# Kernel tuning notes

Measured on AMD Instinct MI355X. Metric: run time of the kernel, lower is better.

## Reference

```python
import jax, jax.numpy as jnp
import numpy as np

B, M, C = 8, 1024, 4096
OP_DIM, MACH_DIM, HID = 128, 128, 128
LEAKY_SLOPE = 0.01  # torch LeakyReLU default


def setup_inputs() -> dict:
    key = jax.random.key(0)
    ks = jax.random.split(key, 10)
    s = lambda *sh: 1.0 / np.sqrt(sh[0])
    return {
        "operation_features": jax.random.normal(ks[0], (B, C, OP_DIM), jnp.float32),
        "machine_features": jax.random.normal(ks[1], (B, M, MACH_DIM), jnp.float32),
        "type_match_mask": jax.random.randint(ks[2], (B, M, C), 0, 2).astype(jnp.float32),
        "q_w": jax.random.uniform(ks[3], (MACH_DIM, HID), jnp.float32, -s(MACH_DIM), s(MACH_DIM)),
        "q_b": jax.random.uniform(ks[4], (HID,), jnp.float32, -s(MACH_DIM), s(MACH_DIM)),
        "kv_w": jax.random.uniform(ks[5], (OP_DIM, 2 * HID), jnp.float32, -s(OP_DIM), s(OP_DIM)),
        "kv_b": jax.random.uniform(ks[6], (2 * HID,), jnp.float32, -s(OP_DIM), s(OP_DIM)),
        "score_w": jax.random.uniform(ks[7], (2 * HID, 1), jnp.float32, -s(2 * HID), s(2 * HID)),
        "score_b": jax.random.uniform(ks[8], (1,), jnp.float32, -s(2 * HID), s(2 * HID)),
        "out_w": jax.random.uniform(ks[9], (HID, MACH_DIM), jnp.float32, -s(HID), s(HID)),
        "out_b": jnp.zeros((MACH_DIM,), jnp.float32),
    }


def reference(operation_features, machine_features, type_match_mask,
              q_w, q_b, kv_w, kv_b, score_w, score_b, out_w, out_b):
    H = q_w.shape[1]
    q = machine_features @ q_w + q_b                      # [B, M, H]
    kv = operation_features @ kv_w + kv_b                 # [B, C, 2H]
    k, v = kv[..., :H], kv[..., H:]                       # [B, C, H] each
    # score MLP Linear(2H -> 1) on cat([q, k]) == q @ Wq + k @ Wk + b,
    # broadcast over [B, M, C] -> never materialize the [B, M, C, 2H] concat.
    wq, wk = score_w[:H, 0], score_w[H:, 0]
    scores = (q @ wq)[:, :, None] + (k @ wk)[:, None, :] + score_b[0]  # [B, M, C]
    scores = jnp.where(scores >= 0, scores, LEAKY_SLOPE * scores)     # LeakyReLU
    masked = scores * type_match_mask                                  # multiplicative mask (as in source)
    attn = jax.nn.softmax(masked, axis=-1)                             # softmax over operations C
    weighted = jnp.einsum('bmc,bch->bmh', attn, v)                     # [B, M, H]
    return weighted @ out_w + out_b                                    # [B, M, MACH_DIM]
```

## Files before the change

### kernel.cpp

```cpp
#include <hip/hip_runtime.h>
#include <hip/hip_bf16.h>

typedef __attribute__((ext_vector_type(8))) short short8;
typedef __attribute__((ext_vector_type(8))) unsigned short u16x8;
typedef __attribute__((ext_vector_type(4))) unsigned short u16x4;
typedef __attribute__((ext_vector_type(4))) float f32x4;
typedef __attribute__((ext_vector_type(4))) unsigned int u32x4;

#define L2E 1.44269504f

__device__ __forceinline__ unsigned short f2bf(float f){
  unsigned u = __float_as_uint(f);
  u += 0x7fffu + ((u >> 16) & 1u);
  return (unsigned short)(u >> 16);
}
__device__ __forceinline__ unsigned pk_bf16(float lo, float hi){
  unsigned a = __float_as_uint(lo);
  a += 0x7fffu + ((a >> 16) & 1u);
  unsigned b = __float_as_uint(hi);
  b += 0x7fffu + ((b >> 16) & 1u);
  return (a >> 16) | (b & 0xffff0000u);
}

__global__ void prep_vecs(const float* __restrict__ qw, const float* __restrict__ qb,
                          const float* __restrict__ kvw, const float* __restrict__ kvb,
                          const float* __restrict__ scw, const float* __restrict__ scb,
                          float* __restrict__ qv, float* __restrict__ kvv,
                          float* __restrict__ cqck){
  int d = threadIdx.x;
  const float4* qr = (const float4*)(qw + d*128);
  const float4* kr = (const float4*)(kvw + d*256);
  float a = 0.f, c = 0.f;
  #pragma unroll 8
  for (int i = 0; i < 32; ++i){
    float4 q4 = qr[i];
    float4 w4 = *(const float4*)(scw + i*4);
    a = fmaf(q4.x, w4.x, a); a = fmaf(q4.y, w4.y, a);
    a = fmaf(q4.z, w4.z, a); a = fmaf(q4.w, w4.w, a);
    float4 k4 = kr[i];
    float4 v4 = *(const float4*)(scw + 128 + i*4);
    c = fmaf(k4.x, v4.x, c); c = fmaf(k4.y, v4.y, c);
    c = fmaf(k4.z, v4.z, c); c = fmaf(k4.w, v4.w, c);
  }
  qv[d] = a; kvv[d] = c;
  if (d == 0){
    float cq = scb[0], ck = 0.f;
    #pragma unroll 8
    for (int i = 0; i < 32; ++i){
      float4 qb4 = *(const float4*)(qb + i*4);
      float4 w4  = *(const float4*)(scw + i*4);
      float4 kb4 = *(const float4*)(kvb + i*4);
      float4 v4  = *(const float4*)(scw + 128 + i*4);
      cq = fmaf(qb4.x, w4.x, cq); cq = fmaf(qb4.y, w4.y, cq);
      cq = fmaf(qb4.z, w4.z, cq); cq = fmaf(qb4.w, w4.w, cq);
      ck = fmaf(kb4.x, v4.x, ck); ck = fmaf(kb4.y, v4.y, ck);
      ck = fmaf(kb4.z, v4.z, ck); ck = fmaf(kb4.w, v4.w, ck);
    }
    cqck[0] = cq; cqck[1] = ck;
  }
}

__global__ __launch_bounds__(256) void prep_w2(const float* __restrict__ kvw,
                          const float* __restrict__ kvb,
                          const float* __restrict__ outw, const float* __restrict__ outb,
                          unsigned short* __restrict__ w2t, float* __restrict__ c2){
  int blk = blockIdx.x;
  if (blk < 64){
    int idx = blk*256 + threadIdx.x;
    int di = idx >> 7, ho = idx & 127;
    const float* kr = kvw + di*256 + 128;
    float s = 0.f;
    for (int h = 0; h < 128; ++h) s = fmaf(kr[h], outw[h*128 + ho], s);
    w2t[ho*128 + di] = f2bf(s);
  } else if (threadIdx.x < 128){
    int ho = threadIdx.x;
    float s = outb[ho];
    for (int h = 0; h < 128; ++h) s = fmaf(kvb[128 + h], outw[h*128 + ho], s);
    c2[ho] = s;
  }
}

__global__ __launch_bounds__(256) void prep_sq(const float* __restrict__ mf,
                          const float* __restrict__ qv, const float* __restrict__ cqck,
                          float* __restrict__ sqp){
  int row = blockIdx.x*4 + (threadIdx.x >> 6);
  int lane = threadIdx.x & 63;
  float s = mf[row*128 + lane] * qv[lane] + mf[row*128 + 64 + lane] * qv[64 + lane];
  #pragma unroll
  for (int o = 32; o; o >>= 1) s += __shfl_xor(s, o, 64);
  if (lane == 0) sqp[row] = L2E * (s + cqck[0]);
}

__global__ __launch_bounds__(256) void prep_sk_tr(const float* __restrict__ of,
                          const float* __restrict__ kvv, const float* __restrict__ cqck,
                          float* __restrict__ skp, unsigned short* __restrict__ ofTk){
  __shared__ unsigned short tile[64*130];
  int b  = blockIdx.x >> 6;
  int c0 = (blockIdx.x & 63) << 6;
  int t  = threadIdx.x;
  int r  = t >> 2, dq = (t & 3) << 5;
  const float* src = of + ((size_t)(b*4096 + c0 + r))*128 + dq;
  float part = 0.f;
  #pragma unroll
  for (int j = 0; j < 32; j += 4){
    float4 v = *(const float4*)(src + j);
    part = fmaf(v.x, kvv[dq + j],     part);
    part = fmaf(v.y, kvv[dq + j + 1], part);
    part = fmaf(v.z, kvv[dq + j + 2], part);
    part = fmaf(v.w, kvv[dq + j + 3], part);
    tile[r*130 + dq + j]     = f2bf(v.x);
    tile[r*130 + dq + j + 1] = f2bf(v.y);
    tile[r*130 + dq + j + 2] = f2bf(v.z);
    tile[r*130 + dq + j + 3] = f2bf(v.w);
  }
  part += __shfl_xor(part, 1, 64);
  part += __shfl_xor(part, 2, 64);
  if ((t & 3) == 0) skp[b*4096 + c0 + r] = L2E * (part + cqck[1]);
  __syncthreads();
  int d = t >> 1, chh = (t & 1) << 5;
  #pragma unroll
  for (int j = 0; j < 4; ++j){
    int cg = c0 + chh + j*8;
    int ksg = cg >> 5, l4g = (cg >> 3) & 3;
    u16x8 v;
    #pragma unroll
    for (int k = 0; k < 8; ++k) v[k] = tile[(chh + j*8 + k)*130 + d];
    *(u16x8*)(ofTk + (((size_t)(b*128 + ksg)*4 + l4g)*128 + d)*8) = v;
  }
}


#define ISSUE_M(MS, KS) { M##MS##a = *(const float4*)(mbase + (KS)*32);          \
                          M##MS##b = *(const float4*)(mbase + (KS)*32 + 4); }
#define ISSUE_S(SS, KS) { S##SS##a = *(const float4*)(sbase + (KS)*32);          \
                          S##SS##b = *(const float4*)(sbase + (KS)*32 + 4); }
#define ISSUE_B(BS, KS) {                                                        \
  const unsigned short* bp = bbase + (size_t)(KS)*4096;                          \
  B##BS##_0 = *(const short8*)(bp);        B##BS##_1 = *(const short8*)(bp+128); \
  B##BS##_2 = *(const short8*)(bp+256);    B##BS##_3 = *(const short8*)(bp+384); \
  B##BS##_4 = *(const short8*)(bp+512);    B##BS##_5 = *(const short8*)(bp+640); \
  B##BS##_6 = *(const short8*)(bp+768);    B##BS##_7 = *(const short8*)(bp+896); }

#define KSTEP(KS, MS, BS, PFB, PFM)                                              \
{                                                                                \
  float sx[8] = {S##BS##a.x,S##BS##a.y,S##BS##a.z,S##BS##a.w,                    \
                 S##BS##b.x,S##BS##b.y,S##BS##b.z,S##BS##b.w};                   \
  float mx[8] = {M##MS##a.x,M##MS##a.y,M##MS##a.z,M##MS##a.w,                    \
                 M##MS##b.x,M##MS##b.y,M##MS##b.z,M##MS##b.w};                   \
  float pv[8];                                                                   \
  _Pragma("unroll")                                                              \
  for (int j = 0; j < 8; ++j){                                                   \
    float s = sqv + sx[j];                  \
    s = fmaxf(s, 0.01f*s);                   \
    s *= mx[j];                                        \
    pv[j] = __builtin_amdgcn_exp2f(s);                                           \
  }                                                                              \
  u32x4 pk;                                                                      \
  pk[0] = pk_bf16(pv[0], pv[1]);                                                 \
  pk[1] = pk_bf16(pv[2], pv[3]);                                                 \
  pk[2] = pk_bf16(pv[4], pv[5]);                                                 \
  pk[3] = pk_bf16(pv[6], pv[7]);                                                 \
  short8 pa = __builtin_bit_cast(short8, pk);                                    \
  accS = __builtin_amdgcn_mfma_f32_16x16x32_bf16(pa, ones, accS, 0, 0, 0);       \
  acc0 = __builtin_amdgcn_mfma_f32_16x16x32_bf16(pa, B##BS##_0, acc0, 0, 0, 0);  \
  acc1 = __builtin_amdgcn_mfma_f32_16x16x32_bf16(pa, B##BS##_1, acc1, 0, 0, 0);  \
  acc2 = __builtin_amdgcn_mfma_f32_16x16x32_bf16(pa, B##BS##_2, acc2, 0, 0, 0);  \
  acc3 = __builtin_amdgcn_mfma_f32_16x16x32_bf16(pa, B##BS##_3, acc3, 0, 0, 0);  \
  acc4 = __builtin_amdgcn_mfma_f32_16x16x32_bf16(pa, B##BS##_4, acc4, 0, 0, 0);  \
  acc5 = __builtin_amdgcn_mfma_f32_16x16x32_bf16(pa, B##BS##_5, acc5, 0, 0, 0);  \
  acc6 = __builtin_amdgcn_mfma_f32_16x16x32_bf16(pa, B##BS##_6, acc6, 0, 0, 0);  \
  acc7 = __builtin_amdgcn_mfma_f32_16x16x32_bf16(pa, B##BS##_7, acc7, 0, 0, 0);  \
  if (PFB){ ISSUE_B(BS, (KS)+2); ISSUE_S(BS, (KS)+2); }                          \
  if (PFM){ ISSUE_M(MS, (KS)+4); }                                              \
}

template<int CSL2>
__global__ __launch_bounds__(256, 2) void attn_main(
    const float* __restrict__ mask, const float* __restrict__ sqp,
    const float* __restrict__ skp, const unsigned short* __restrict__ ofTk,
    float* __restrict__ pacc, float* __restrict__ prs)
{
  constexpr int CS = 1 << CSL2;
  constexpr int NK = 128 >> CSL2;
  const int t = threadIdx.x, w = t >> 6, l = t & 63;
  const int l15 = l & 15, l4 = l >> 4;
  const int unit = blockIdx.x*4 + w;
  const int cs   = unit & (CS - 1);
  const int bmt  = unit >> CSL2;
  const int b    = bmt >> 6;
  const int m0   = (bmt & 63) << 4;
  const int c0   = cs << (12 - CSL2);

  const int grow = b*1024 + m0 + l15;
  const float sqv = sqp[grow];
  const float* mbase = mask + (size_t)grow*4096 + c0 + l4*8;
  const float* sbase = skp + b*4096 + c0 + l4*8;
  const unsigned short* bbase =
      ofTk + (((size_t)(b*128 + (c0 >> 5))*4 + l4)*128 + l15)*8;

  const short one_bf = (short)0x3F80;
  const short8 ones = {one_bf,one_bf,one_bf,one_bf,one_bf,one_bf,one_bf,one_bf};

  f32x4 acc0={0,0,0,0},acc1={0,0,0,0},acc2={0,0,0,0},acc3={0,0,0,0},
        acc4={0,0,0,0},acc5={0,0,0,0},acc6={0,0,0,0},acc7={0,0,0,0},
        accS={0,0,0,0};
  float4 M0a,M0b,M1a,M1b,M2a,M2b,M3a,M3b;
  float4 S0a,S0b,S1a,S1b;
  short8 B0_0,B0_1,B0_2,B0_3,B0_4,B0_5,B0_6,B0_7;
  short8 B1_0,B1_1,B1_2,B1_3,B1_4,B1_5,B1_6,B1_7;

  ISSUE_M(0, 0); ISSUE_S(0, 0);
  ISSUE_B(0, 0);
  ISSUE_M(1, 1); ISSUE_S(1, 1);
  ISSUE_B(1, 1);
  ISSUE_M(2, 2); ISSUE_M(3, 3);

  for (int g = 0; g < NK/4 - 1; ++g){
    const int ks = g*4;
    KSTEP(ks+0, 0, 0, true, true);
    KSTEP(ks+1, 1, 1, true, true);
    KSTEP(ks+2, 2, 0, true, true);
    KSTEP(ks+3, 3, 1, true, true);
  }
  KSTEP(NK-4, 0, 0, true,  false);
  KSTEP(NK-3, 1, 1, true,  false);
  KSTEP(NK-2, 2, 0, false, false);
  KSTEP(NK-1, 3, 1, false, false);

  if (l15 == 0) *(f32x4*)(prs + unit*16 + l4*4) = accS;

  float* po = pacc + (size_t)unit*2048 + l15*16 + l4*4;
  *(f32x4*)(po + 0*256) = acc0;  *(f32x4*)(po + 1*256) = acc1;
  *(f32x4*)(po + 2*256) = acc2;  *(f32x4*)(po + 3*256) = acc3;
  *(f32x4*)(po + 4*256) = acc4;  *(f32x4*)(po + 5*256) = acc5;
  *(f32x4*)(po + 6*256) = acc6;  *(f32x4*)(po + 7*256) = acc7;
}

__global__ __launch_bounds__(256) void reduce_gemm2(
    const float* __restrict__ pacc, const float* __restrict__ prs,
    const unsigned short* __restrict__ w2t, const float* __restrict__ c2,
    float* __restrict__ out, int csl2)
{
  __shared__ unsigned short A2[64*128];
  __shared__ float rs[64];
  const int bmt64 = blockIdx.x;
  const int b = bmt64 >> 4, mt = bmt64 & 15;
  const int CS = 1 << csl2;
  const int t = threadIdx.x;

  f32x4 a[8];
  #pragma unroll
  for (int i = 0; i < 8; ++i) a[i] = {0.f,0.f,0.f,0.f};
  for (int cs = 0; cs < CS; ++cs){
    #pragma unroll
    for (int i = 0; i < 8; ++i){
      const int flat = (i*256 + t)*4;
      const int q = flat >> 11, f2 = flat & 2047;
      const float* pb = pacc + ((size_t)((bmt64*4 + q)*CS + cs))*2048 + f2;
      f32x4 v = *(const f32x4*)pb;
      a[i][0]+=v[0]; a[i][1]+=v[1]; a[i][2]+=v[2]; a[i][3]+=v[3];
    }
  }
  if (t < 64){
    float s = 0.f;
    const int q = t >> 4, r16 = t & 15;
    for (int cs = 0; cs < CS; ++cs) s += prs[((bmt64*4 + q)*CS + cs)*16 + r16];
    rs[t] = 1.f / s;
  }
  __syncthreads();
  #pragma unroll
  for (int i = 0; i < 8; ++i){
    const int flat = (i*256 + t)*4;
    const int q = flat >> 11, f2 = flat & 2047;
    const int col = f2 >> 4, r16 = f2 & 15;
    #pragma unroll
    for (int k = 0; k < 4; ++k){
      const int row = q*16 + r16 + k;
      unsigned short h = f2bf(a[i][k] * rs[row]);
      *(unsigned short*)((char*)A2 + row*256 + ((col*2) ^ ((row & 7) << 4))) = h;
    }
  }
  __syncthreads();

  const int w = t >> 6, l = t & 63, l15 = l & 15, l4 = l >> 4;
  f32x4 o[4][2];
  #pragma unroll
  for (int mf = 0; mf < 4; ++mf){ o[mf][0] = {0.f,0.f,0.f,0.f}; o[mf][1] = {0.f,0.f,0.f,0.f}; }
  const unsigned short* wp0 = w2t + (size_t)(w*32 + l15)*128 + l4*8;
  const char* ab = (const char*)A2 + l15*256;
  const int xa = (l15 & 7) << 4;
  #pragma unroll
  for (int ks = 0; ks < 4; ++ks){
    short8 b0 = *(const short8*)(wp0 + ks*32);
    short8 b1 = *(const short8*)(wp0 + 16*128 + ks*32);
    #pragma unroll
    for (int mf = 0; mf < 4; ++mf){
      short8 af = *(const short8*)(ab + mf*4096 + ((ks*64 + l4*16) ^ xa));
      o[mf][0] = __builtin_amdgcn_mfma_f32_16x16x32_bf16(af, b0, o[mf][0], 0, 0, 0);
      o[mf][1] = __builtin_amdgcn_mfma_f32_16x16x32_bf16(af, b1, o[mf][1], 0, 0, 0);
    }
  }
  #pragma unroll
  for (int mf = 0; mf < 4; ++mf)
    #pragma unroll
    for (int n = 0; n < 2; ++n){
      const int col = w*32 + n*16 + l15;
      const float cc = c2[col];
      #pragma unroll
      for (int j = 0; j < 4; ++j){
        const int row = mf*16 + l4*4 + j;
        out[((size_t)(b*1024 + mt*64 + row))*128 + col] = o[mf][n][j] + cc;
      }
    }
}

extern "C" void kernel_launch(void* const* d_in, const int* in_sizes, int n_in,
                              void* d_out, int out_size, void* d_ws, size_t ws_size,
                              hipStream_t stream){
  const float* of   = (const float*)d_in[0];
  const float* mf   = (const float*)d_in[1];
  const float* mask = (const float*)d_in[2];
  const float* qw   = (const float*)d_in[3];
  const float* qb   = (const float*)d_in[4];
  const float* kvw  = (const float*)d_in[5];
  const float* kvb  = (const float*)d_in[6];
  const float* scw  = (const float*)d_in[7];
  const float* scb  = (const float*)d_in[8];
  const float* outw = (const float*)d_in[9];
  const float* outb = (const float*)d_in[10];
  float* out = (float*)d_out;

  char* ws = (char*)d_ws;
  unsigned short* ofTk = (unsigned short*)(ws);
  unsigned short* w2t  = (unsigned short*)(ws + 8388608);
  float* c2   = (float*)(ws + 8421376);
  float* sqp  = (float*)(ws + 8421888);
  float* skp  = (float*)(ws + 8454656);
  float* qv   = (float*)(ws + 8585728);
  float* kvv  = (float*)(ws + 8586240);
  float* cqck = (float*)(ws + 8586752);
  const size_t fixed_end = 8587008;

  int csl2 = 2;
  while (csl2 > 1){
    size_t nunit = (size_t)512 << csl2;
    if (fixed_end + nunit*16*4 + nunit*2048*4 <= ws_size) break;
    --csl2;
  }
  size_t nunit = (size_t)512 << csl2;
  float* prs  = (float*)(ws + fixed_end);
  float* pacc = (float*)(ws + fixed_end + nunit*16*4);
  int nblk = (int)(nunit >> 2);

  prep_vecs<<<1, 128, 0, stream>>>(qw, qb, kvw, kvb, scw, scb, qv, kvv, cqck);
  prep_w2<<<65, 256, 0, stream>>>(kvw, kvb, outw, outb, w2t, c2);
  prep_sq<<<2048, 256, 0, stream>>>(mf, qv, cqck, sqp);
  prep_sk_tr<<<512, 256, 0, stream>>>(of, kvv, cqck, skp, ofTk);
  if (csl2 == 2)
    attn_main<2><<<nblk, 256, 0, stream>>>(mask, sqp, skp, ofTk, pacc, prs);
  else
    attn_main<1><<<nblk, 256, 0, stream>>>(mask, sqp, skp, ofTk, pacc, prs);
  reduce_gemm2<<<128, 256, 0, stream>>>(pacc, prs, w2t, c2, out, csl2);
}
```

Before: 75.87 us.

## Stream mask and key scores through LDS via async global-to-LDS loads

The main attention kernel now stages the mask tiles in a 4-deep per-wave LDS ring and the per-column key scores in LDS, filled with global_load_lds direct copies and paced by explicit vmcnt waits. The B operand is loaded per step instead of double-buffered in registers, which frees registers so occupancy can go from 2 to 4 blocks per CU. The column split is raised from 4 to 8 slices, which gives more units and more partial results to reduce. The risks are fragile hand-tuned waitcnt values, extra LDS traffic, and a larger partial-sum buffer and reduction.

```diff
diff --git a/kernel.cpp b/kernel.cpp
--- a/kernel.cpp
+++ b/kernel.cpp
@@ -20,6 +20,11 @@
   unsigned b = __float_as_uint(hi);
   b += 0x7fffu + ((b >> 16) & 1u);
   return (a >> 16) | (b & 0xffff0000u);
+}
+__device__ __forceinline__ void gl_lds16(const void* g, void* l){
+  __builtin_amdgcn_global_load_lds(
+      (const __attribute__((address_space(1))) unsigned*)g,
+      (__attribute__((address_space(3))) unsigned*)l, 16, 0, 0);
 }
 
 __global__ void prep_vecs(const float* __restrict__ qw, const float* __restrict__ qb,
@@ -130,23 +135,30 @@
 }
 
 
-#define ISSUE_M(MS, KS) { M##MS##a = *(const float4*)(mbase + (KS)*32);          \
-                          M##MS##b = *(const float4*)(mbase + (KS)*32 + 4); }
-#define ISSUE_S(SS, KS) { S##SS##a = *(const float4*)(sbase + (KS)*32);          \
-                          S##SS##b = *(const float4*)(sbase + (KS)*32 + 4); }
-#define ISSUE_B(BS, KS) {                                                        \
+#define WVAL(KS) ((KS)==0 ? 0 : (KS)==1 ? 10 : (KS)==2 ? 20 : \
+                  ((KS) >= NK-3 ? (24 + 2*(NK-1-(KS))) : 30))
+
+#define KSTEP(KS) if ((KS) < NK) {                                               \
+  asm volatile("s_waitcnt vmcnt(%0)" :: "i"(WVAL(KS)) : "memory");               \
+  __builtin_amdgcn_sched_barrier(0);                                             \
   const unsigned short* bp = bbase + (size_t)(KS)*4096;                          \
-  B##BS##_0 = *(const short8*)(bp);        B##BS##_1 = *(const short8*)(bp+128); \
-  B##BS##_2 = *(const short8*)(bp+256);    B##BS##_3 = *(const short8*)(bp+384); \
-  B##BS##_4 = *(const short8*)(bp+512);    B##BS##_5 = *(const short8*)(bp+640); \
-  B##BS##_6 = *(const short8*)(bp+768);    B##BS##_7 = *(const short8*)(bp+896); }
-
-#define KSTEP(KS, MS, BS, PFB, PFM)                                              \
-{                                                                                \
-  float sx[8] = {S##BS##a.x,S##BS##a.y,S##BS##a.z,S##BS##a.w,                    \
-                 S##BS##b.x,S##BS##b.y,S##BS##b.z,S##BS##b.w};                   \
-  float mx[8] = {M##MS##a.x,M##MS##a.y,M##MS##a.z,M##MS##a.w,                    \
-                 M##MS##b.x,M##MS##b.y,M##MS##b.z,M##MS##b.w};                   \
+  short8 b0 = *(const short8*)(bp);       short8 b1 = *(const short8*)(bp+128);  \
+  short8 b2 = *(const short8*)(bp+256);   short8 b3 = *(const short8*)(bp+384);  \
+  short8 b4 = *(const short8*)(bp+512);   short8 b5 = *(const short8*)(bp+640);  \
+  short8 b6 = *(const short8*)(bp+768);   short8 b7 = *(const short8*)(bp+896);  \
+  const char* ms = Mring + ((KS)&3)*2048;                                        \
+  f32x4 m0v = *(const f32x4*)(ms + lB);                                          \
+  f32x4 m1v = *(const f32x4*)(ms + 1024 + lB);                                   \
+  f32x4 s0v = *(const f32x4*)(Sl + (KS)*128 + l4*32);                            \
+  f32x4 s1v = *(const f32x4*)(Sl + (KS)*128 + l4*32 + 16);                       \
+  asm volatile("s_waitcnt lgkmcnt(0)" ::: "memory");                             \
+  __builtin_amdgcn_sched_barrier(0);                                             \
+  if ((KS)+4 < NK){                                                              \
+    gl_lds16(mrow + ((KS)+4)*32,     Mring + (((KS)+4)&3)*2048);                 \
+    gl_lds16(mrow + ((KS)+4)*32 + 4, Mring + (((KS)+4)&3)*2048 + 1024);          \
+  }                                                                              \
+  float sx[8] = {s0v[0],s0v[1],s0v[2],s0v[3],s1v[0],s1v[1],s1v[2],s1v[3]};       \
+  float mx[8] = {m0v[0],m0v[1],m0v[2],m0v[3],m1v[0],m1v[1],m1v[2],m1v[3]};       \
   float pv[8];                                                                   \
   _Pragma("unroll")                                                              \
   for (int j = 0; j < 8; ++j){                                                   \
@@ -155,35 +167,36 @@
     s *= mx[j];                                        \
     pv[j] = __builtin_amdgcn_exp2f(s);                                           \
   }                                                                              \
-  u32x4 pk;                                                                      \
-  pk[0] = pk_bf16(pv[0], pv[1]);                                                 \
-  pk[1] = pk_bf16(pv[2], pv[3]);                                                 \
-  pk[2] = pk_bf16(pv[4], pv[5]);                                                 \
-  pk[3] = pk_bf16(pv[6], pv[7]);                                                 \
-  short8 pa = __builtin_bit_cast(short8, pk);                                    \
+  u32x4 pkv;                                                                     \
+  pkv[0] = pk_bf16(pv[0], pv[1]);  pkv[1] = pk_bf16(pv[2], pv[3]);               \
+  pkv[2] = pk_bf16(pv[4], pv[5]);  pkv[3] = pk_bf16(pv[6], pv[7]);               \
+  short8 pa = __builtin_bit_cast(short8, pkv);                                   \
   accS = __builtin_amdgcn_mfma_f32_16x16x32_bf16(pa, ones, accS, 0, 0, 0);       \
-  acc0 = __builtin_amdgcn_mfma_f32_16x16x32_bf16(pa, B##BS##_0, acc0, 0, 0, 0);  \
-  acc1 = __builtin_amdgcn_mfma_f32_16x16x32_bf16(pa, B##BS##_1, acc1, 0, 0, 0);  \
-  acc2 = __builtin_amdgcn_mfma_f32_16x16x32_bf16(pa, B##BS##_2, acc2, 0, 0, 0);  \
-  acc3 = __builtin_amdgcn_mfma_f32_16x16x32_bf16(pa, B##BS##_3, acc3, 0, 0, 0);  \
-  acc4 = __builtin_amdgcn_mfma_f32_16x16x32_bf16(pa, B##BS##_4, acc4, 0, 0, 0);  \
-  acc5 = __builtin_amdgcn_mfma_f32_16x16x32_bf16(pa, B##BS##_5, acc5, 0, 0, 0);  \
-  acc6 = __builtin_amdgcn_mfma_f32_16x16x32_bf16(pa, B##BS##_6, acc6, 0, 0, 0);  \
-  acc7 = __builtin_amdgcn_mfma_f32_16x16x32_bf16(pa, B##BS##_7, acc7, 0, 0, 0);  \
-  if (PFB){ ISSUE_B(BS, (KS)+2); ISSUE_S(BS, (KS)+2); }                          \
-  if (PFM){ ISSUE_M(MS, (KS)+4); }                                              \
+  acc0 = __builtin_amdgcn_mfma_f32_16x16x32_bf16(pa, b0, acc0, 0, 0, 0);         \
+  acc1 = __builtin_amdgcn_mfma_f32_16x16x32_bf16(pa, b1, acc1, 0, 0, 0);         \
+  acc2 = __builtin_amdgcn_mfma_f32_16x16x32_bf16(pa, b2, acc2, 0, 0, 0);         \
+  acc3 = __builtin_amdgcn_mfma_f32_16x16x32_bf16(pa, b3, acc3, 0, 0, 0);         \
+  acc4 = __builtin_amdgcn_mfma_f32_16x16x32_bf16(pa, b4, acc4, 0, 0, 0);         \
+  acc5 = __builtin_amdgcn_mfma_f32_16x16x32_bf16(pa, b5, acc5, 0, 0, 0);         \
+  acc6 = __builtin_amdgcn_mfma_f32_16x16x32_bf16(pa, b6, acc6, 0, 0, 0);         \
+  acc7 = __builtin_amdgcn_mfma_f32_16x16x32_bf16(pa, b7, acc7, 0, 0, 0);         \
 }
 
 template<int CSL2>
-__global__ __launch_bounds__(256, 2) void attn_main(
+__global__ __launch_bounds__(256, 4) void attn_main(
     const float* __restrict__ mask, const float* __restrict__ sqp,
     const float* __restrict__ skp, const unsigned short* __restrict__ ofTk,
     float* __restrict__ pacc, float* __restrict__ prs)
 {
   constexpr int CS = 1 << CSL2;
   constexpr int NK = 128 >> CSL2;
+  constexpr int SBYTES = (4096 >> CSL2) * 4;
+  constexpr int SINSTS = SBYTES / 1024;
+  __shared__ char lds[4][4*2048 + SBYTES];
+
   const int t = threadIdx.x, w = t >> 6, l = t & 63;
   const int l15 = l & 15, l4 = l >> 4;
+  const int lB = l * 16;
   const int unit = blockIdx.x*4 + w;
   const int cs   = unit & (CS - 1);
   const int bmt  = unit >> CSL2;
@@ -191,10 +204,13 @@
   const int m0   = (bmt & 63) << 4;
   const int c0   = cs << (12 - CSL2);
 
+  char* Mring = &lds[w][0];
+  char* Sl    = &lds[w][8192];
+
   const int grow = b*1024 + m0 + l15;
   const float sqv = sqp[grow];
-  const float* mbase = mask + (size_t)grow*4096 + c0 + l4*8;
-  const float* sbase = skp + b*4096 + c0 + l4*8;
+  const float* mrow = mask + (size_t)grow*4096 + c0 + l4*8;
+  const float* srow = skp + b*4096 + c0;
   const unsigned short* bbase =
       ofTk + (((size_t)(b*128 + (c0 >> 5))*4 + l4)*128 + l15)*8;
 
@@ -204,28 +220,20 @@
   f32x4 acc0={0,0,0,0},acc1={0,0,0,0},acc2={0,0,0,0},acc3={0,0,0,0},
         acc4={0,0,0,0},acc5={0,0,0,0},acc6={0,0,0,0},acc7={0,0,0,0},
         accS={0,0,0,0};
-  float4 M0a,M0b,M1a,M1b,M2a,M2b,M3a,M3b;
-  float4 S0a,S0b,S1a,S1b;
-  short8 B0_0,B0_1,B0_2,B0_3,B0_4,B0_5,B0_6,B0_7;
-  short8 B1_0,B1_1,B1_2,B1_3,B1_4,B1_5,B1_6,B1_7;
-
-  ISSUE_M(0, 0); ISSUE_S(0, 0);
-  ISSUE_B(0, 0);
-  ISSUE_M(1, 1); ISSUE_S(1, 1);
-  ISSUE_B(1, 1);
-  ISSUE_M(2, 2); ISSUE_M(3, 3);
-
-  for (int g = 0; g < NK/4 - 1; ++g){
-    const int ks = g*4;
-    KSTEP(ks+0, 0, 0, true, true);
-    KSTEP(ks+1, 1, 1, true, true);
-    KSTEP(ks+2, 2, 0, true, true);
-    KSTEP(ks+3, 3, 1, true, true);
-  }
-  KSTEP(NK-4, 0, 0, true,  false);
-  KSTEP(NK-3, 1, 1, true,  false);
-  KSTEP(NK-2, 2, 0, false, false);
-  KSTEP(NK-1, 3, 1, false, false);
+
+  #pragma unroll
+  for (int i = 0; i < SINSTS; ++i)
+    gl_lds16(srow + l*4 + i*256, Sl + i*1024);
+  #pragma unroll
+  for (int p = 0; p < 4; ++p){
+    gl_lds16(mrow + p*32,     Mring + p*2048);
+    gl_lds16(mrow + p*32 + 4, Mring + p*2048 + 1024);
+  }
+
+  KSTEP(0)  KSTEP(1)  KSTEP(2)  KSTEP(3)  KSTEP(4)  KSTEP(5)  KSTEP(6)  KSTEP(7)
+  KSTEP(8)  KSTEP(9)  KSTEP(10) KSTEP(11) KSTEP(12) KSTEP(13) KSTEP(14) KSTEP(15)
+  KSTEP(16) KSTEP(17) KSTEP(18) KSTEP(19) KSTEP(20) KSTEP(21) KSTEP(22) KSTEP(23)
+  KSTEP(24) KSTEP(25) KSTEP(26) KSTEP(27) KSTEP(28) KSTEP(29) KSTEP(30) KSTEP(31)
 
   if (l15 == 0) *(f32x4*)(prs + unit*16 + l4*4) = accS;
 
@@ -341,8 +349,8 @@
   float* cqck = (float*)(ws + 8586752);
   const size_t fixed_end = 8587008;
 
-  int csl2 = 2;
-  while (csl2 > 1){
+  int csl2 = 3;
+  while (csl2 > 2){
     size_t nunit = (size_t)512 << csl2;
     if (fixed_end + nunit*16*4 + nunit*2048*4 <= ws_size) break;
     --csl2;
@@ -356,9 +364,9 @@
   prep_w2<<<65, 256, 0, stream>>>(kvw, kvb, outw, outb, w2t, c2);
   prep_sq<<<2048, 256, 0, stream>>>(mf, qv, cqck, sqp);
   prep_sk_tr<<<512, 256, 0, stream>>>(of, kvv, cqck, skp, ofTk);
-  if (csl2 == 2)
+  if (csl2 == 3)
+    attn_main<3><<<nblk, 256, 0, stream>>>(mask, sqp, skp, ofTk, pacc, prs);
+  else
     attn_main<2><<<nblk, 256, 0, stream>>>(mask, sqp, skp, ofTk, pacc, prs);
-  else
-    attn_main<1><<<nblk, 256, 0, stream>>>(mask, sqp, skp, ofTk, pacc, prs);
   reduce_gemm2<<<128, 256, 0, stream>>>(pacc, prs, w2t, c2, out, csl2);
 }
```

Result: slower. 110.2 us (+45.2%).
